# Kernel optimization log

Measured on AMD Instinct MI355X. Metric: run time of the kernel, lower is better.

Reference implementation:

```python
import jax, jax.numpy as jnp
import numpy as np

B, T, D = 4, 1024, 1024
H, DH = 16, 64
FFN = 4096
CAPACITY = 0.25
C_VAR = 1.0
BETA_CE = 1.0
BETA_CU = 1.0
EPS = 1e-6


def _rmsnorm(x, w, eps=EPS):
    v = jnp.mean(jnp.square(x), axis=-1, keepdims=True)
    return x * jax.lax.rsqrt(v + eps) * w


def _rope(x, pos):
    # x: [B, S, H, DH], pos: [B, S] float positions
    half = x.shape[-1] // 2
    inv = 1.0 / (10000.0 ** (jnp.arange(half, dtype=jnp.float32) / half))
    ang = pos[:, :, None] * inv                      # [B, S, half]
    cos = jnp.cos(ang)[:, :, None, :]                # [B, S, 1, half]
    sin = jnp.sin(ang)[:, :, None, :]
    x1, x2 = x[..., :half], x[..., half:]
    return jnp.concatenate([x1 * cos - x2 * sin, x2 * cos + x1 * sin], axis=-1)


def _decoder(x, pos, ln1, wq, wk, wv, wo, ln2, wg, wu, wd):
    # Qwen2-style decoder layer: RMSNorm -> rotary causal MHA -> res -> RMSNorm -> SwiGLU -> res
    b, s, d = x.shape
    h = _rmsnorm(x, ln1)
    q = _rope((h @ wq).reshape(b, s, H, DH), pos)
    k = _rope((h @ wk).reshape(b, s, H, DH), pos)
    v = (h @ wv).reshape(b, s, H, DH)
    scores = jnp.einsum('bqhd,bkhd->bhqk', q, k) / jnp.sqrt(jnp.float32(DH))
    causal = jnp.tril(jnp.ones((s, s), dtype=bool))
    scores = jnp.where(causal, scores, jnp.finfo(scores.dtype).min)
    attn = jax.nn.softmax(scores, axis=-1)
    o = jnp.einsum('bhqk,bkhd->bqhd', attn, v).reshape(b, s, d) @ wo
    x = x + o
    h2 = _rmsnorm(x, ln2)
    return x + (jax.nn.silu(h2 @ wg) * (h2 @ wu)) @ wd


def _forward(hidden_states, ln1_1, wq1, wk1, wv1, wo1, ln2_1, wg1, wu1, wd1,
             ln1_2, wq2, wk2, wv2, wo2, ln2_2, wg2, wu2, wd2,
             prior_norm_w, prior_w):
    b, t, d = hidden_states.shape
    pos = jnp.broadcast_to(jnp.arange(t, dtype=jnp.float32)[None, :], (b, t))
    # decision layer: full-sequence decoder block
    processed = _decoder(hidden_states, pos, ln1_1, wq1, wk1, wv1, wo1, ln2_1, wg1, wu1, wd1)
    res = processed - hidden_states                  # actual_residual
    # prior network: RMSNorm + linear -> (mu_q, log_var_q)
    prior_h = _rmsnorm(hidden_states, prior_norm_w)
    mu_logvar = prior_h @ prior_w                    # [B, T, 2D]
    mu, logvar = mu_logvar[..., :d], mu_logvar[..., d:]
    # surprise router signals
    d_st = jnp.mean(jnp.square(res), axis=-1)        # [B, T]
    d_ch = jnp.mean(0.5 * (logvar - jnp.log(C_VAR)
                           + (C_VAR + jnp.square(res - mu)) * jnp.exp(-logvar) - 1.0), axis=-1)
    g = jax.nn.sigmoid(BETA_CE * (d_st - jnp.mean(d_st)) + BETA_CU * (d_ch - jnp.mean(d_ch)))
    # top-k selection, sorted by token index (as in the torch code)
    k_sel = max(1, int(t * CAPACITY))
    scores, idx = jax.lax.top_k(g, k_sel)            # [B, k]
    order = jnp.argsort(idx, axis=-1)
    idx = jnp.take_along_axis(idx, order, axis=-1)
    scores = jnp.take_along_axis(scores, order, axis=-1)
    # gather -> decoder layer on selected tokens -> soft-gated scatter back
    bidx = jnp.arange(b)[:, None]
    sel = processed[bidx, idx]                       # [B, k, D]
    y = _decoder(sel, idx.astype(jnp.float32), ln1_2, wq2, wk2, wv2, wo2, ln2_2, wg2, wu2, wd2)
    upd = sel + scores[..., None] * (y - sel)        # soft gating of the block residual
    return processed.at[bidx, idx].set(upd)


def setup_inputs():
    key = jax.random.key(0)
    ks = jax.random.split(key, 16)
    s = 0.02

    def w(k, shape):
        return jax.random.normal(k, shape, dtype=jnp.float32) * s

    inp = {'hidden_states': jax.random.normal(ks[0], (B, T, D), dtype=jnp.float32)}
    for i, n in enumerate(['wq1', 'wk1', 'wv1', 'wo1', 'wq2', 'wk2', 'wv2', 'wo2']):
        inp[n] = w(ks[1 + i], (D, D))
    inp['wg1'] = w(ks[9], (D, FFN)); inp['wu1'] = w(ks[10], (D, FFN)); inp['wd1'] = w(ks[11], (FFN, D))
    inp['wg2'] = w(ks[12], (D, FFN)); inp['wu2'] = w(ks[13], (D, FFN)); inp['wd2'] = w(ks[14], (FFN, D))
    for n in ['ln1_1', 'ln2_1', 'ln1_2', 'ln2_2', 'prior_norm_w']:
        inp[n] = jnp.ones((D,), dtype=jnp.float32)
    inp['prior_w'] = w(ks[15], (D, 2 * D))
    return inp


def reference(hidden_states, ln1_1, wq1, wk1, wv1, wo1, ln2_1, wg1, wu1, wd1,
              ln1_2, wq2, wk2, wv2, wo2, ln2_2, wg2, wu2, wd2,
              prior_norm_w, prior_w):
    return _forward(hidden_states, ln1_1, wq1, wk1, wv1, wo1, ln2_1, wg1, wu1, wd1,
                    ln1_2, wq2, wk2, wv2, wo2, ln2_2, wg2, wu2, wd2,
                    prior_norm_w, prior_w)
```

## Files before the change

### kernel.cpp

```cpp
#include <hip/hip_runtime.h>
#include <math.h>

#define Bdim 4
#define Tdim 1024
#define Ddim 1024
#define Hdim 16
#define DHdim 64
#define FFNdim 4096
#define KSEL 256
#define EPSf 1e-6f

typedef __attribute__((ext_vector_type(8))) short bf16x8;
typedef __attribute__((ext_vector_type(4))) float f32x4;
typedef __attribute__((ext_vector_type(4))) unsigned int u32x4;
typedef unsigned short ushort_t;

#define MFMA_BF16(a,b,c) __builtin_amdgcn_mfma_f32_16x16x32_bf16(a,b,c,0,0,0)

__device__ __forceinline__ int clamp_row(int r){ return r < 0 ? 0 : (r > Tdim-1 ? Tdim-1 : r); }

__device__ __forceinline__ void split8(const float* xs, u32x4* hi, u32x4* lo){
  unsigned int hm[8], lm[8];
  #pragma unroll
  for (int i=0;i<8;i++){
// ... 164 lines not shown
  }
  float m_i[4], l_i[4];
  f32x4 oacc[4];
  #pragma unroll
  for (int r=0;r<4;r++){ m_i[r] = -3.4e38f; l_i[r] = 0.f; }
  #pragma unroll
  for (int fd=0;fd<4;fd++){ f32x4 z = {0.f,0.f,0.f,0.f}; oacc[fd] = z; }
  float* Pw = Pds + wv*(16*68);
  for (int j0 = 0; j0 <= q0; j0 += 64){
    __syncthreads();
    {
      int row = tid >> 2;
      int s0 = (tid & 3)*2;
      const float* kp = k + (((size_t)b*S + j0 + row)*Hdim + h)*64 + s0*8;
      #pragma unroll
      for (int g=0; g<2; g++){
        int slot = s0 + g;
        float xs[8];
        #pragma unroll
        for (int i=0;i<8;i++) xs[i] = kp[g*8 + i];
        u32x4 hi, lo; split8(xs, &hi, &lo);
        int base = row*64 + ((slot ^ (row&7))*8);
        *(u32x4*)&Kh[base] = hi;
        *(u32x4*)&Kl[base] = lo;
      }
    }
    {
      int j = tid & 31;
      int dbase = (tid >> 5)*8;
      const float* vp0 = v + (((size_t)b*S + j0 + 2*j)*Hdim + h)*64 + dbase;
      const float* vp1 = vp0 + (size_t)Hdim*64;
      float x0[8], x1[8];
      #pragma unroll
      for (int i=0;i<8;i++){ x0[i]=vp0[i]; x1[i]=vp1[i]; }
      unsigned int* VhW = (unsigned int*)Vh;
      unsigned int* VlW = (unsigned int*)Vl;
      #pragma unroll
      for (int i=0;i<8;i++){
        int d = dbase + i;
        unsigned int h0,l0,h1,l1;
        split1(x0[i], &h0, &l0); split1(x1[i], &h1, &l1);
        int off = d*32 + (((j>>2) ^ (d&7))*4) + (j&3);
        VhW[off] = h0 | (h1<<16);
        VlW[off] = l0 | (l1<<16);
      }
    }
    __syncthreads();
    f32x4 sacc[4];
    #pragma unroll
    for (int fj=0;fj<4;fj++){ f32x4 z = {0.f,0.f,0.f,0.f}; sacc[fj] = z; }
    #pragma unroll
    for (int ks=0; ks<2; ks++){
      #pragma unroll
      for (int fj=0;fj<4;fj++){
        int kr = fj*16 + ln15;
        int idx = kr*64 + (((ks*4+lk) ^ (kr&7))*8);
        bf16x8 kb_h = *(const bf16x8*)&Kh[idx];
        bf16x8 kb_l = *(const bf16x8*)&Kl[idx];
        sacc[fj] = MFMA_BF16(qa_h[ks], kb_h, sacc[fj]);
        sacc[fj] = MFMA_BF16(qa_h[ks], kb_l, sacc[fj]);
        sacc[fj] = MFMA_BF16(qa_l[ks], kb_h, sacc[fj]);
      }
    }
    #pragma unroll
    for (int fj=0;fj<4;fj++){
      int key = j0 + fj*16 + ln15;
      #pragma unroll
      for (int r=0;r<4;r++){
        float sv = sacc[fj][r]*0.125f;
        int qrow = q0 + qbase + lk*4 + r;
        sacc[fj][r] = (key > qrow) ? -3.4e38f : sv;
      }
    }
    float p[4][4];
    #pragma unroll
    for (int r=0;r<4;r++){
      float mt = fmaxf(fmaxf(sacc[0][r],sacc[1][r]), fmaxf(sacc[2][r],sacc[3][r]));
      #pragma unroll
      for (int off=1; off<16; off<<=1) mt = fmaxf(mt, __shfl_xor(mt, off));
      float m_new = fmaxf(m_i[r], mt);
      float alpha = expf(m_i[r] - m_new);
      float rs = 0.f;
      #pragma unroll
      for (int fj=0;fj<4;fj++){
        p[fj][r] = expf(sacc[fj][r] - m_new);
        rs += p[fj][r];
      }
      #pragma unroll
      for (int off=1; off<16; off<<=1) rs += __shfl_xor(rs, off);
      l_i[r] = l_i[r]*alpha + rs;
      m_i[r] = m_new;
      #pragma unroll
      for (int fd=0;fd<4;fd++) oacc[fd][r] *= alpha;
    }
    #pragma unroll
    for (int fj=0;fj<4;fj++)
      #pragma unroll
      for (int r=0;r<4;r++)
        Pw[(lk*4+r)*68 + fj*16 + ln15] = p[fj][r];
    #pragma unroll
    for (int ks=0; ks<2; ks++){
      f32x4 pf0 = *(const f32x4*)&Pw[ln15*68 + ks*32 + lk*8];
      f32x4 pf1 = *(const f32x4*)&Pw[ln15*68 + ks*32 + lk*8 + 4];
      float xs[8] = {pf0[0],pf0[1],pf0[2],pf0[3],pf1[0],pf1[1],pf1[2],pf1[3]};
      u32x4 hi, lo; split8(xs, &hi, &lo);
      bf16x8 pa_h = *(bf16x8*)&hi;
      bf16x8 pa_l = *(bf16x8*)&lo;
      #pragma unroll
      for (int fd=0;fd<4;fd++){
        int d = fd*16 + ln15;
        int idx = d*64 + (((ks*4+lk) ^ (d&7))*8);
        bf16x8 vb_h = *(const bf16x8*)&Vh[idx];
        bf16x8 vb_l = *(const bf16x8*)&Vl[idx];
        oacc[fd] = MFMA_BF16(pa_h, vb_h, oacc[fd]);
        oacc[fd] = MFMA_BF16(pa_h, vb_l, oacc[fd]);
        oacc[fd] = MFMA_BF16(pa_l, vb_h, oacc[fd]);
      }
    }
  }
  #pragma unroll
  for (int r=0;r<4;r++){
    float inv_l = 1.0f/l_i[r];
    #pragma unroll
    for (int fd=0;fd<4;fd++){
      o[(((size_t)b*S + q0 + qbase + lk*4 + r)*Hdim + h)*64 + fd*16 + ln15] = oacc[fd][r]*inv_l;
    }
  }
}

__global__ __launch_bounds__(256) void k_attn_ps(
    const ushort_t* __restrict__ Qph, const ushort_t* __restrict__ Qpl,
    const ushort_t* __restrict__ Kph, const ushort_t* __restrict__ Kpl,
    const ushort_t* __restrict__ Vph, const ushort_t* __restrict__ Vpl,
    ushort_t* __restrict__ Oh, ushort_t* __restrict__ Ol, int S){
  __shared__ ushort_t Kh[64*64], Kl[64*64];
  __shared__ ushort_t Vh[64*64], Vl[64*64];
  __shared__ float Pds[4*16*68];
  const int qt = blockIdx.x, h = blockIdx.y, b = blockIdx.z;
  const int q0 = qt*64;
  const int tid = threadIdx.x;
  const int lane = tid & 63;
  const int ln15 = lane & 15, lk = lane >> 4;
  const int wv = tid >> 6;
  const int qbase = wv*16;
  bf16x8 qa_h[2], qa_l[2];
  {
    size_t qoff = (((size_t)b*S + q0 + qbase + ln15)*Hdim + h)*64;
    #pragma unroll
    for (int ks=0; ks<2; ks++){
      qa_h[ks] = *(const bf16x8*)&Qph[qoff + ks*32 + lk*8];
      qa_l[ks] = *(const bf16x8*)&Qpl[qoff + ks*32 + lk*8];
    }
  }
  float m_i[4], l_i[4];
  f32x4 oacc[4];
  #pragma unroll
  for (int r=0;r<4;r++){ m_i[r] = -3.4e38f; l_i[r] = 0.f; }
  #pragma unroll
  for (int fd=0;fd<4;fd++){ f32x4 z = {0.f,0.f,0.f,0.f}; oacc[fd] = z; }
  float* Pw = Pds + wv*(16*68);
  for (int j0 = 0; j0 <= q0; j0 += 64){
    __syncthreads();
    #pragma unroll
    for (int g=0; g<2; g++){
      int row = g*32 + (tid >> 3);
      int ks = tid & 7;
      size_t ga = (((size_t)b*S + j0 + row)*Hdim + h)*64 + ks*8;
      u32x4 hi = *(const u32x4*)&Kph[ga];
      u32x4 lo = *(const u32x4*)&Kpl[ga];
      int base = row*64 + ((ks ^ (row&7))*8);
      *(u32x4*)&Kh[base] = hi;
      *(u32x4*)&Kl[base] = lo;
    }
    {
      int j = tid & 31;
      int dbase = (tid >> 5)*8;
      size_t g0 = (((size_t)b*S + j0 + 2*j)*Hdim + h)*64 + dbase;
      size_t g1 = g0 + (size_t)Hdim*64;
      u32x4 ah = *(const u32x4*)&Vph[g0];
      u32x4 bh = *(const u32x4*)&Vph[g1];
      u32x4 al = *(const u32x4*)&Vpl[g0];
      u32x4 bl = *(const u32x4*)&Vpl[g1];
      unsigned int* VhW = (unsigned int*)Vh;
      unsigned int* VlW = (unsigned int*)Vl;
      #pragma unroll
      for (int i=0;i<4;i++){
        int d0 = dbase + 2*i, d1 = d0 + 1;
        int off0 = d0*32 + (((j>>2) ^ (d0&7))*4) + (j&3);
        int off1 = d1*32 + (((j>>2) ^ (d1&7))*4) + (j&3);
        VhW[off0] = (ah[i] & 0xFFFFu) | (bh[i] << 16);
        VhW[off1] = (ah[i] >> 16)     | (bh[i] & 0xFFFF0000u);
        VlW[off0] = (al[i] & 0xFFFFu) | (bl[i] << 16);
        VlW[off1] = (al[i] >> 16)     | (bl[i] & 0xFFFF0000u);
      }
    }
    __syncthreads();
    f32x4 sacc[4];
    #pragma unroll
    for (int fj=0;fj<4;fj++){ f32x4 z = {0.f,0.f,0.f,0.f}; sacc[fj] = z; }
    #pragma unroll
    for (int ks=0; ks<2; ks++){
      #pragma unroll
      for (int fj=0;fj<4;fj++){
        int kr = fj*16 + ln15;
        int idx = kr*64 + (((ks*4+lk) ^ (kr&7))*8);
        bf16x8 kb_h = *(const bf16x8*)&Kh[idx];
        bf16x8 kb_l = *(const bf16x8*)&Kl[idx];
        sacc[fj] = MFMA_BF16(qa_h[ks], kb_h, sacc[fj]);
        sacc[fj] = MFMA_BF16(qa_h[ks], kb_l, sacc[fj]);
        sacc[fj] = MFMA_BF16(qa_l[ks], kb_h, sacc[fj]);
      }
    }
    #pragma unroll
    for (int fj=0;fj<4;fj++){
      int key = j0 + fj*16 + ln15;
      #pragma unroll
      for (int r=0;r<4;r++){
        float sv = sacc[fj][r]*0.125f;
        int qrow = q0 + qbase + lk*4 + r;
        sacc[fj][r] = (key > qrow) ? -3.4e38f : sv;
      }
    }
    float p[4][4];
    #pragma unroll
    for (int r=0;r<4;r++){
      float mt = fmaxf(fmaxf(sacc[0][r],sacc[1][r]), fmaxf(sacc[2][r],sacc[3][r]));
      #pragma unroll
      for (int off=1; off<16; off<<=1) mt = fmaxf(mt, __shfl_xor(mt, off));
      float m_new = fmaxf(m_i[r], mt);
      float alpha = expf(m_i[r] - m_new);
      float rs = 0.f;
      #pragma unroll
      for (int fj=0;fj<4;fj++){
        p[fj][r] = expf(sacc[fj][r] - m_new);
        rs += p[fj][r];
      }
      #pragma unroll
      for (int off=1; off<16; off<<=1) rs += __shfl_xor(rs, off);
      l_i[r] = l_i[r]*alpha + rs;
      m_i[r] = m_new;
      #pragma unroll
      for (int fd=0;fd<4;fd++) oacc[fd][r] *= alpha;
    }
    #pragma unroll
    for (int fj=0;fj<4;fj++)
      #pragma unroll
      for (int r=0;r<4;r++)
        Pw[(lk*4+r)*68 + fj*16 + ln15] = p[fj][r];
    #pragma unroll
    for (int ks=0; ks<2; ks++){
      f32x4 pf0 = *(const f32x4*)&Pw[ln15*68 + ks*32 + lk*8];
      f32x4 pf1 = *(const f32x4*)&Pw[ln15*68 + ks*32 + lk*8 + 4];
      float xs[8] = {pf0[0],pf0[1],pf0[2],pf0[3],pf1[0],pf1[1],pf1[2],pf1[3]};
      u32x4 hi, lo; split8(xs, &hi, &lo);
      bf16x8 pa_h = *(bf16x8*)&hi;
      bf16x8 pa_l = *(bf16x8*)&lo;
      #pragma unroll
      for (int fd=0;fd<4;fd++){
        int d = fd*16 + ln15;
        int idx = d*64 + (((ks*4+lk) ^ (d&7))*8);
        bf16x8 vb_h = *(const bf16x8*)&Vh[idx];
        bf16x8 vb_l = *(const bf16x8*)&Vl[idx];
        oacc[fd] = MFMA_BF16(pa_h, vb_h, oacc[fd]);
        oacc[fd] = MFMA_BF16(pa_h, vb_l, oacc[fd]);
        oacc[fd] = MFMA_BF16(pa_l, vb_h, oacc[fd]);
      }
    }
  }
  #pragma unroll
  for (int r=0;r<4;r++){
    float inv_l = 1.0f/l_i[r];
    #pragma unroll
    for (int fd=0;fd<4;fd++){
      float val = oacc[fd][r]*inv_l;
      unsigned int h16,l16; split1(val,&h16,&l16);
      size_t cix = (((size_t)b*S + q0 + qbase + lk*4 + r)*Hdim + h)*64 + fd*16 + ln15;
      Oh[cix] = (ushort_t)h16;
      Ol[cix] = (ushort_t)l16;
    }
  }
}

__global__ __launch_bounds__(256) void k_gemm_mfma(
    const float* __restrict__ A, const float* __restrict__ W,
    float* __restrict__ C, const float* __restrict__ addv,
    int K, int ldw, int ldc){
  __shared__ ushort_t Ah[128*32], Al[128*32], Bh[128*32], Bl[128*32];
  const int tid = threadIdx.x;
  const int row0 = blockIdx.y*128, col0 = blockIdx.x*128;
  const int lane = tid & 63;
  const int ln15 = lane & 15, lk = lane >> 4;
  const int wv = tid >> 6;
  const int wrow0 = (wv >> 1)*64, wcol0 = (wv & 1)*64;
  const int arow = tid >> 2;
  const int aks  = tid & 3;
  const int bcol = tid & 127;
  const int bks0 = tid >> 7;
  f32x4 acc[4][4];
  #pragma unroll
  for (int i=0;i<4;i++)
    #pragma unroll
    for (int j=0;j<4;j++){ f32x4 z = {0.f,0.f,0.f,0.f}; acc[i][j] = z; }
  for (int k0 = 0; k0 < K; k0 += 32){
    #pragma unroll
    for (int g=0; g<2; g++){
      int row = g*64 + arow;
      const float* ap = A + (size_t)(row0+row)*K + k0 + aks*8;
      float xs[8];
      #pragma unroll
      for (int i=0;i<8;i++) xs[i] = ap[i];
      u32x4 hi, lo; split8(xs, &hi, &lo);
      int base = row*32 + ((aks ^ ((row>>1)&3))*8);
      *(u32x4*)&Ah[base] = hi;
      *(u32x4*)&Al[base] = lo;
    }
    #pragma unroll
    for (int g=0; g<2; g++){
      int ks = bks0 + 2*g;
      const float* wp = W + (size_t)(k0 + ks*8)*ldw + col0 + bcol;
      float xs[8];
      #pragma unroll
      for (int i=0;i<8;i++) xs[i] = wp[(size_t)i*ldw];
      u32x4 hi, lo; split8(xs, &hi, &lo);
      int base = bcol*32 + ((ks ^ ((bcol>>1)&3))*8);
      *(u32x4*)&Bh[base] = hi;
      *(u32x4*)&Bl[base] = lo;
    }
    __syncthreads();
    bf16x8 ah[4], al[4];
    #pragma unroll
    for (int fi=0;fi<4;fi++){
      int r = wrow0 + fi*16 + ln15;
      int idx = r*32 + ((lk ^ ((r>>1)&3))*8);
      ah[fi] = *(const bf16x8*)&Ah[idx];
      al[fi] = *(const bf16x8*)&Al[idx];
    }
    #pragma unroll
    for (int fj=0;fj<4;fj++){
      int c = wcol0 + fj*16 + ln15;
      int idx = c*32 + ((lk ^ ((c>>1)&3))*8);
      bf16x8 bh = *(const bf16x8*)&Bh[idx];
      bf16x8 bl = *(const bf16x8*)&Bl[idx];
      #pragma unroll
      for (int fi=0;fi<4;fi++){
        acc[fi][fj] = MFMA_BF16(ah[fi], bh, acc[fi][fj]);
        acc[fi][fj] = MFMA_BF16(ah[fi], bl, acc[fi][fj]);
        acc[fi][fj] = MFMA_BF16(al[fi], bh, acc[fi][fj]);
      }
    }
    __syncthreads();
  }
  #pragma unroll
  for (int fi=0;fi<4;fi++){
    #pragma unroll
    for (int fj=0;fj<4;fj++){
      f32x4 v = acc[fi][fj];
      int cc = col0 + wcol0 + fj*16 + ln15;
      #pragma unroll
      for (int r=0;r<4;r++){
        size_t cix = (size_t)(row0 + wrow0 + fi*16 + lk*4 + r)*ldc + cc;
        float val = v[r];
        if (addv) val += addv[cix];
        C[cix] = val;
      }
    }
  }
}

__global__ __launch_bounds__(512) void k_gemm_ps(
    const ushort_t* __restrict__ Ahp, const ushort_t* __restrict__ Alp, int lda,
    const ushort_t* __restrict__ Bhp, const ushort_t* __restrict__ Blp, int ldb,
    float* __restrict__ C, ushort_t* __restrict__ Chp, ushort_t* __restrict__ Clp,
    const float* __restrict__ addv, int K, int ldc){
  __shared__ ushort_t Ah[128*32], Al[128*32], Bh[128*32], Bl[128*32];
  const int tid = threadIdx.x;
  const int row0 = blockIdx.y*128, col0 = blockIdx.x*128;
  const int lane = tid & 63;
  const int ln15 = lane & 15, lk = lane >> 4;
  const int wv = tid >> 6;
  const int wrow0 = (wv >> 2)*64, wcol0 = (wv & 3)*32;
  const int t8 = tid >> 2, ks4 = tid & 3;
  const int sbase = t8*32 + ((ks4 ^ ((t8>>1)&3))*8);
  const size_t gaBase = (size_t)(row0 + t8)*lda + ks4*8;
  const size_t gbBase = (size_t)(col0 + t8)*ldb + ks4*8;

  f32x4 acc[4][2];
  #pragma unroll
  for (int i=0;i<4;i++)
    #pragma unroll
    for (int j=0;j<2;j++){ f32x4 z = {0.f,0.f,0.f,0.f}; acc[i][j] = z; }

  u32x4 rAh = *(const u32x4*)&Ahp[gaBase];
  u32x4 rAl = *(const u32x4*)&Alp[gaBase];
  u32x4 rBh = *(const u32x4*)&Bhp[gbBase];
  u32x4 rBl = *(const u32x4*)&Blp[gbBase];

  for (int k0 = 0; k0 < K; k0 += 32){
    __syncthreads();
    *(u32x4*)&Ah[sbase] = rAh;
    *(u32x4*)&Al[sbase] = rAl;
    *(u32x4*)&Bh[sbase] = rBh;
    *(u32x4*)&Bl[sbase] = rBl;
    __syncthreads();
    if (k0 + 32 < K){
      rAh = *(const u32x4*)&Ahp[gaBase + k0 + 32];
      rAl = *(const u32x4*)&Alp[gaBase + k0 + 32];
      rBh = *(const u32x4*)&Bhp[gbBase + k0 + 32];
      rBl = *(const u32x4*)&Blp[gbBase + k0 + 32];
    }
    bf16x8 ah[4], al[4];
    #pragma unroll
    for (int fi=0;fi<4;fi++){
      int r = wrow0 + fi*16 + ln15;
      int idx = r*32 + ((lk ^ ((r>>1)&3))*8);
      ah[fi] = *(const bf16x8*)&Ah[idx];
      al[fi] = *(const bf16x8*)&Al[idx];
    }
    #pragma unroll
    for (int fj=0;fj<2;fj++){
      int c = wcol0 + fj*16 + ln15;
      int idx = c*32 + ((lk ^ ((c>>1)&3))*8);
      bf16x8 bh = *(const bf16x8*)&Bh[idx];
      bf16x8 bl = *(const bf16x8*)&Bl[idx];
      #pragma unroll
      for (int fi=0;fi<4;fi++){
        acc[fi][fj] = MFMA_BF16(ah[fi], bh, acc[fi][fj]);
        acc[fi][fj] = MFMA_BF16(ah[fi], bl, acc[fi][fj]);
        acc[fi][fj] = MFMA_BF16(al[fi], bh, acc[fi][fj]);
      }
    }
  }
  if (Chp){
    #pragma unroll
    for (int fi=0;fi<4;fi++){
      #pragma unroll
      for (int fj=0;fj<2;fj++){
        f32x4 v = acc[fi][fj];
        int cc = col0 + wcol0 + fj*16 + ln15;
        #pragma unroll
        for (int r=0;r<4;r++){
          size_t cix = (size_t)(row0 + wrow0 + fi*16 + lk*4 + r)*ldc + cc;
          unsigned int h16,l16; split1(v[r],&h16,&l16);
          Chp[cix] = (ushort_t)h16;
          Clp[cix] = (ushort_t)l16;
        }
      }
    }
  } else {
    #pragma unroll
    for (int fi=0;fi<4;fi++){
      #pragma unroll
      for (int fj=0;fj<2;fj++){
        f32x4 v = acc[fi][fj];
        int cc = col0 + wcol0 + fj*16 + ln15;
        #pragma unroll
        for (int r=0;r<4;r++){
          size_t cix = (size_t)(row0 + wrow0 + fi*16 + lk*4 + r)*ldc + cc;
          float val = v[r];
          if (addv) val += addv[cix];
          C[cix] = val;
        }
      }
    }
  }
}

__global__ __launch_bounds__(256) void k_gemm_dual_mfma(
    const float* __restrict__ A, const float* __restrict__ Wg,
    const float* __restrict__ Wu, float* __restrict__ C,
    int K, int ldw, int ldc){
  __shared__ ushort_t Ah[128*32], Al[128*32];
  __shared__ ushort_t Gh[64*32], Gl[64*32], Uh[64*32], Ul[64*32];
  const int tid = threadIdx.x;
  const int row0 = blockIdx.y*128, col0 = blockIdx.x*64;
  const int lane = tid & 63;
  const int ln15 = lane & 15, lk = lane >> 4;
  const int wv = tid >> 6;
  const int wrow0 = (wv >> 1)*64, wcol0 = (wv & 1)*32;
  const int arow = tid >> 2;
  const int aks  = tid & 3;
  const int bcol = tid & 63;
  const int bks  = tid >> 6;
  f32x4 ag[4][2], au[4][2];
  #pragma unroll
  for (int i=0;i<4;i++)
    #pragma unroll
    for (int j=0;j<2;j++){ f32x4 z = {0.f,0.f,0.f,0.f}; ag[i][j] = z; au[i][j] = z; }
  for (int k0 = 0; k0 < K; k0 += 32){
    #pragma unroll
    for (int g=0; g<2; g++){
      int row = g*64 + arow;
      const float* ap = A + (size_t)(row0+row)*K + k0 + aks*8;
      float xs[8];
      #pragma unroll
      for (int i=0;i<8;i++) xs[i] = ap[i];
      u32x4 hi, lo; split8(xs, &hi, &lo);
      int base = row*32 + ((aks ^ ((row>>1)&3))*8);
      *(u32x4*)&Ah[base] = hi;
      *(u32x4*)&Al[base] = lo;
    }
    {
      int wbase = bcol*32 + ((bks ^ ((bcol>>1)&3))*8);
      const float* gp = Wg + (size_t)(k0 + bks*8)*ldw + col0 + bcol;
      float xs[8];
      #pragma unroll
      for (int i=0;i<8;i++) xs[i] = gp[(size_t)i*ldw];
      u32x4 hi, lo; split8(xs, &hi, &lo);
      *(u32x4*)&Gh[wbase] = hi;
      *(u32x4*)&Gl[wbase] = lo;
      const float* up = Wu + (size_t)(k0 + bks*8)*ldw + col0 + bcol;
      #pragma unroll
      for (int i=0;i<8;i++) xs[i] = up[(size_t)i*ldw];
      split8(xs, &hi, &lo);
      *(u32x4*)&Uh[wbase] = hi;
      *(u32x4*)&Ul[wbase] = lo;
    }
    __syncthreads();
    bf16x8 ah[4], al[4];
    #pragma unroll
    for (int fi=0;fi<4;fi++){
      int r = wrow0 + fi*16 + ln15;
      int idx = r*32 + ((lk ^ ((r>>1)&3))*8);
      ah[fi] = *(const bf16x8*)&Ah[idx];
      al[fi] = *(const bf16x8*)&Al[idx];
    }
    #pragma unroll
    for (int fj=0;fj<2;fj++){
      int c = wcol0 + fj*16 + ln15;
      int idx = c*32 + ((lk ^ ((c>>1)&3))*8);
      bf16x8 gh = *(const bf16x8*)&Gh[idx];
      bf16x8 gl = *(const bf16x8*)&Gl[idx];
      bf16x8 uh = *(const bf16x8*)&Uh[idx];
      bf16x8 ul = *(const bf16x8*)&Ul[idx];
      #pragma unroll
      for (int fi=0;fi<4;fi++){
        ag[fi][fj] = MFMA_BF16(ah[fi], gh, ag[fi][fj]);
        ag[fi][fj] = MFMA_BF16(ah[fi], gl, ag[fi][fj]);
        ag[fi][fj] = MFMA_BF16(al[fi], gh, ag[fi][fj]);
        au[fi][fj] = MFMA_BF16(ah[fi], uh, au[fi][fj]);
        au[fi][fj] = MFMA_BF16(ah[fi], ul, au[fi][fj]);
        au[fi][fj] = MFMA_BF16(al[fi], uh, au[fi][fj]);
      }
    }
    __syncthreads();
  }
  #pragma unroll
  for (int fi=0;fi<4;fi++){
    #pragma unroll
    for (int fj=0;fj<2;fj++){
      f32x4 vg = ag[fi][fj];
      f32x4 vu = au[fi][fj];
      int cc = col0 + wcol0 + fj*16 + ln15;
      #pragma unroll
      for (int r=0;r<4;r++){
        size_t cix = (size_t)(row0 + wrow0 + fi*16 + lk*4 + r)*ldc + cc;
        float gg = vg[r];
        C[cix] = (gg/(1.0f+expf(-gg))) * vu[r];
      }
    }
  }
}

__global__ __launch_bounds__(512) void k_gemm_dual_ps(
    const ushort_t* __restrict__ Ahp, const ushort_t* __restrict__ Alp, int lda,
    const ushort_t* __restrict__ Ghp, const ushort_t* __restrict__ Glp,
    const ushort_t* __restrict__ Uhp, const ushort_t* __restrict__ Ulp, int ldb,
    ushort_t* __restrict__ Chp, ushort_t* __restrict__ Clp, int K, int ldc){
  __shared__ ushort_t Ah[128*32], Al[128*32];
  __shared__ ushort_t Gh[64*32], Gl[64*32], Uh[64*32], Ul[64*32];
  const int tid = threadIdx.x;
  const int row0 = blockIdx.y*128, col0 = blockIdx.x*64;
  const int lane = tid & 63;
  const int ln15 = lane & 15, lk = lane >> 4;
  const int wv = tid >> 6;
  const int wrow0 = (wv >> 1)*32, wcol0 = (wv & 1)*32;
  const int t8 = tid >> 2, ks4 = tid & 3;
  const int abase = t8*32 + ((ks4 ^ ((t8>>1)&3))*8);
  const size_t gaBase = (size_t)(row0 + t8)*lda + ks4*8;
  const int isU = (tid >= 256);
  const int t2 = tid & 255;
  const int wcolS = t2 >> 2, wksS = t2 & 3;
  const int wsbase = wcolS*32 + ((wksS ^ ((wcolS>>1)&3))*8);
  const ushort_t* Wph = isU ? Uhp : Ghp;
  const ushort_t* Wpl = isU ? Ulp : Glp;
  ushort_t* WsH = isU ? Uh : Gh;
  ushort_t* WsL = isU ? Ul : Gl;
  const size_t gwBase = (size_t)(col0 + wcolS)*ldb + wksS*8;

  f32x4 ag[2][2], au[2][2];
  #pragma unroll
  for (int i=0;i<2;i++)
    #pragma unroll
    for (int j=0;j<2;j++){ f32x4 z = {0.f,0.f,0.f,0.f}; ag[i][j] = z; au[i][j] = z; }

  u32x4 rAh = *(const u32x4*)&Ahp[gaBase];
  u32x4 rAl = *(const u32x4*)&Alp[gaBase];
  u32x4 rWh = *(const u32x4*)&Wph[gwBase];
  u32x4 rWl = *(const u32x4*)&Wpl[gwBase];

  for (int k0 = 0; k0 < K; k0 += 32){
    __syncthreads();
    *(u32x4*)&Ah[abase] = rAh;
    *(u32x4*)&Al[abase] = rAl;
    *(u32x4*)&WsH[wsbase] = rWh;
    *(u32x4*)&WsL[wsbase] = rWl;
    __syncthreads();
    if (k0 + 32 < K){
      rAh = *(const u32x4*)&Ahp[gaBase + k0 + 32];
      rAl = *(const u32x4*)&Alp[gaBase + k0 + 32];
      rWh = *(const u32x4*)&Wph[gwBase + k0 + 32];
      rWl = *(const u32x4*)&Wpl[gwBase + k0 + 32];
    }
    bf16x8 ah[2], al[2];
// ... 90 lines not shown
                        float* __restrict__ g){
  int tid = threadIdx.x;
  float s1=0.f, s2=0.f;
  for (int i=tid; i<Bdim*Tdim; i+=1024){ s1+=dst[i]; s2+=dch[i]; }
  __shared__ float r1[1024], r2[1024];
  r1[tid]=s1; r2[tid]=s2; __syncthreads();
  for (int st=512; st>0; st>>=1){ if(tid<st){r1[tid]+=r1[tid+st]; r2[tid]+=r2[tid+st];} __syncthreads(); }
  float m1 = r1[0]/(float)(Bdim*Tdim), m2 = r2[0]/(float)(Bdim*Tdim);
  for (int i=tid; i<Bdim*Tdim; i+=1024){
    float z = (dst[i]-m1) + (dch[i]-m2);
    g[i] = 1.0f/(1.0f+expf(-z));
  }
}

__global__ __launch_bounds__(1024) void k_select(const float* __restrict__ g, int* __restrict__ selidx,
                         float* __restrict__ selsc){
  int b = blockIdx.x, t = threadIdx.x;
  __shared__ float gs[1024];
  __shared__ int flag[1024];
  float gv = g[b*Tdim + t];
  if (!(gv == gv)) gv = -3.4e38f;
  gs[t] = gv; __syncthreads();
  float gi = gs[t];
  int rank = 0;
  for (int j=0;j<Tdim;j++){
    float gj = gs[j];
    rank += (gj > gi) || (gj == gi && j < t);
  }
  int sel = (rank < KSEL) ? 1 : 0;
  flag[t] = sel; __syncthreads();
  if (sel){
    int pos = 0;
    for (int j=0;j<t;j++) pos += flag[j];
    if (pos < KSEL){
      selidx[b*KSEL+pos] = t;
      selsc[b*KSEL+pos] = gi;
    }
  }
}

__global__ __launch_bounds__(256) void k_gather(const float* __restrict__ proc, const int* __restrict__ selidx,
                         float* __restrict__ sel){
  int j = blockIdx.x, b = blockIdx.y, tid = threadIdx.x;
  int row = clamp_row(selidx[b*KSEL+j]);
  const float* src = proc + ((size_t)b*Tdim + row)*Ddim;
  float* dst = sel + ((size_t)b*KSEL + j)*Ddim;
  for (int d=tid; d<Ddim; d+=256) dst[d]=src[d];
}

__global__ void k_out(const float* __restrict__ proc, float* __restrict__ out, int n){
  int i = blockIdx.x*blockDim.x + threadIdx.x;
  if (i<n) out[i] = proc[i];
}

__global__ __launch_bounds__(256) void k_scatter(const float* __restrict__ sel, const float* __restrict__ y,
                          const float* __restrict__ selsc, const int* __restrict__ selidx,
                          float* __restrict__ out){
  int j = blockIdx.x, b = blockIdx.y, tid = threadIdx.x;
  int row = clamp_row(selidx[b*KSEL+j]);
  float s = selsc[b*KSEL+j];
  const float* sp = sel + ((size_t)b*KSEL + j)*Ddim;
  const float* yp = y + ((size_t)b*KSEL + j)*Ddim;
  float* op = out + ((size_t)b*Tdim + row)*Ddim;
  for (int d=tid; d<Ddim; d+=256){
    op[d] = sp[d] + s*(yp[d]-sp[d]);
  }
}

extern "C" void kernel_launch(void* const* d_in, const int* in_sizes, int n_in,
                              void* d_out, int out_size, void* d_ws, size_t ws_size,
                              hipStream_t stream){
  (void)in_sizes; (void)n_in; (void)out_size;
  const float* hidden = (const float*)d_in[0];
  const float* wq1 = (const float*)d_in[1];
  const float* wk1 = (const float*)d_in[2];
  const float* wv1 = (const float*)d_in[3];
  const float* wo1 = (const float*)d_in[4];
  const float* wq2 = (const float*)d_in[5];
  const float* wk2 = (const float*)d_in[6];
  const float* wv2 = (const float*)d_in[7];
  const float* wo2 = (const float*)d_in[8];
  const float* wg1 = (const float*)d_in[9];
  const float* wu1 = (const float*)d_in[10];
  const float* wd1 = (const float*)d_in[11];
  const float* wg2 = (const float*)d_in[12];
  const float* wu2 = (const float*)d_in[13];
  const float* wd2 = (const float*)d_in[14];
  const float* ln1_1 = (const float*)d_in[15];
  const float* ln2_1 = (const float*)d_in[16];
  const float* ln1_2 = (const float*)d_in[17];
  const float* ln2_2 = (const float*)d_in[18];
  const float* prior_norm = (const float*)d_in[19];
  const float* prior_w = (const float*)d_in[20];

  const size_t A = (size_t)Bdim*Tdim*Ddim;
  const size_t Q = (size_t)Bdim*KSEL*Ddim;
  const int n = (int)A;
  const int MT = Bdim*Tdim;
  const int M2 = Bdim*KSEL;

  const size_t WELEMS = 34u*1024*1024;
  size_t need_old = (4*A + 16384) * sizeof(float);
  size_t need_new = need_old + 2*WELEMS*sizeof(ushort_t);

  if (ws_size < need_old){
    k_fallback<<<(n+255)/256,256,0,stream>>>(hidden, (float*)d_out, n);
    return;
  }

  float* ws = (float*)d_ws;
  float* R0 = ws;
  float* R1 = ws + 1*A;
  float* R2 = ws + 2*A;
  float* R3 = ws + 3*A;
  float* dstb = ws + 4*A;
  float* dchb = dstb + 4096;
  float* gb   = dchb + 4096;
  float* selsc= gb + 4096;
  int*   selidx = (int*)(selsc + 1024);

  k_init_sel<<<4,256,0,stream>>>(selidx, selsc, Bdim*KSEL);

  if (ws_size >= need_new){
    ushort_t* wpb = (ushort_t*)(ws + 4*A + 16384);
    size_t cur = 0;
    const size_t M1x1 = (size_t)1024*1024;
    const size_t M1x4 = (size_t)1024*4096;
    #define ALLOCW(nm, KN) ushort_t* nm##_h = wpb + cur; ushort_t* nm##_l = wpb + cur + (KN); cur += 2*(size_t)(KN);
    ALLOCW(pwq1, M1x1) ALLOCW(pwk1, M1x1) ALLOCW(pwv1, M1x1) ALLOCW(pwo1, M1x1)
    ALLOCW(pwq2, M1x1) ALLOCW(pwk2, M1x1) ALLOCW(pwv2, M1x1) ALLOCW(pwo2, M1x1)
    ALLOCW(pwg1, M1x4) ALLOCW(pwu1, M1x4) ALLOCW(pwd1, M1x4)
    ALLOCW(pwg2, M1x4) ALLOCW(pwu2, M1x4) ALLOCW(pwd2, M1x4)
    ALLOCW(ppw, (size_t)2048*1024)
    #undef ALLOCW

    k_split_w<<<dim3(16,16),256,0,stream>>>(wq1, pwq1_h, pwq1_l, 1024, 1024);
    k_split_w<<<dim3(16,16),256,0,stream>>>(wk1, pwk1_h, pwk1_l, 1024, 1024);
    k_split_w<<<dim3(16,16),256,0,stream>>>(wv1, pwv1_h, pwv1_l, 1024, 1024);
    k_split_w<<<dim3(16,16),256,0,stream>>>(wo1, pwo1_h, pwo1_l, 1024, 1024);
    k_split_w<<<dim3(16,16),256,0,stream>>>(wq2, pwq2_h, pwq2_l, 1024, 1024);
    k_split_w<<<dim3(16,16),256,0,stream>>>(wk2, pwk2_h, pwk2_l, 1024, 1024);
    k_split_w<<<dim3(16,16),256,0,stream>>>(wv2, pwv2_h, pwv2_l, 1024, 1024);
    k_split_w<<<dim3(16,16),256,0,stream>>>(wo2, pwo2_h, pwo2_l, 1024, 1024);
    k_split_w<<<dim3(64,16),256,0,stream>>>(wg1, pwg1_h, pwg1_l, 1024, 4096);
    k_split_w<<<dim3(64,16),256,0,stream>>>(wu1, pwu1_h, pwu1_l, 1024, 4096);
    k_split_w<<<dim3(16,64),256,0,stream>>>(wd1, pwd1_h, pwd1_l, 4096, 1024);
    k_split_w<<<dim3(64,16),256,0,stream>>>(wg2, pwg2_h, pwg2_l, 1024, 4096);
    k_split_w<<<dim3(64,16),256,0,stream>>>(wu2, pwu2_h, pwu2_l, 1024, 4096);
    k_split_w<<<dim3(16,64),256,0,stream>>>(wd2, pwd2_h, pwd2_l, 4096, 1024);
    k_split_w<<<dim3(32,16),256,0,stream>>>(prior_w, ppw_h, ppw_l, 1024, 2048);

    ushort_t* Hh = (ushort_t*)R0; ushort_t* Hl = Hh + A;
    k_rmsnorm_sp<<<MT,256,0,stream>>>(hidden, ln1_1, Hh, Hl);
    dim3 gD(Ddim/128, MT/128);
    k_gemm_ps<<<gD,512,0,stream>>>(Hh,Hl,1024, pwq1_h,pwq1_l,1024, R1, nullptr,nullptr, nullptr, 1024, 1024);
    k_gemm_ps<<<gD,512,0,stream>>>(Hh,Hl,1024, pwk1_h,pwk1_l,1024, R2, nullptr,nullptr, nullptr, 1024, 1024);
    ushort_t* Vp_h = (ushort_t*)R3; ushort_t* Vp_l = Vp_h + A;
    k_gemm_ps<<<gD,512,0,stream>>>(Hh,Hl,1024, pwv1_h,pwv1_l,1024, nullptr, Vp_h, Vp_l, nullptr, 1024, 1024);
    int nr = MT*Hdim*32;
    ushort_t* Qp_h = (ushort_t*)R0; ushort_t* Qp_l = Qp_h + A;
    k_rope_sp<<<(nr+255)/256,256,0,stream>>>(R1, nullptr, Tdim, nr, Qp_h, Qp_l);
    ushort_t* Kp_h = (ushort_t*)R1; ushort_t* Kp_l = Kp_h + A;
    k_rope_sp<<<(nr+255)/256,256,0,stream>>>(R2, nullptr, Tdim, nr, Kp_h, Kp_l);
    ushort_t* Op_h = (ushort_t*)R2; ushort_t* Op_l = Op_h + A;
    k_attn_ps<<<dim3(Tdim/64,Hdim,Bdim),256,0,stream>>>(Qp_h,Qp_l, Kp_h,Kp_l, Vp_h,Vp_l, Op_h,Op_l, Tdim);
    k_gemm_ps<<<gD,512,0,stream>>>(Op_h,Op_l,1024, pwo1_h,pwo1_l,1024, R1, nullptr,nullptr, hidden, 1024, 1024);
    ushort_t* H2h = (ushort_t*)R0; ushort_t* H2l = H2h + A;
    k_rmsnorm_sp<<<MT,256,0,stream>>>(R1, ln2_1, H2h, H2l);
    ushort_t* ACTh = (ushort_t*)R3; ushort_t* ACTl = ACTh + A;
    for (int c = 0; c < 4; c++){
      k_gemm_dual_ps<<<dim3(16, MT/128),512,0,stream>>>(H2h,H2l,1024,
          pwg1_h + (size_t)c*M1x1, pwg1_l + (size_t)c*M1x1,
          pwu1_h + (size_t)c*M1x1, pwu1_l + (size_t)c*M1x1, 1024,
          ACTh, ACTl, 1024, 1024);
      k_gemm_ps<<<dim3(8, MT/128),512,0,stream>>>(ACTh,ACTl,1024,
          pwd1_h + (size_t)c*1024, pwd1_l + (size_t)c*1024, 4096,
          R2, nullptr,nullptr, (c==0 ? R1 : R2), 1024, 1024);
    }

    ushort_t* PHh = (ushort_t*)R0; ushort_t* PHl = PHh + A;
    k_rmsnorm_sp<<<MT,256,0,stream>>>(hidden, prior_norm, PHh, PHl);
    k_gemm_ps<<<gD,512,0,stream>>>(PHh,PHl,1024, ppw_h, ppw_l, 1024, R1, nullptr,nullptr, nullptr, 1024, 1024);
    k_gemm_ps<<<gD,512,0,stream>>>(PHh,PHl,1024, ppw_h + M1x1, ppw_l + M1x1, 1024, R3, nullptr,nullptr, nullptr, 1024, 1024);
    k_dstch2<<<MT,256,0,stream>>>(R2, hidden, R1, R3, dstb, dchb);
    k_gate<<<1,1024,0,stream>>>(dstb, dchb, gb);
    k_select<<<Bdim,1024,0,stream>>>(gb, selidx, selsc);
    float* SELX = R0;
    k_gather<<<dim3(KSEL,Bdim),256,0,stream>>>(R2, selidx, SELX);

    ushort_t* h2h = (ushort_t*)R1;        ushort_t* h2l = h2h + Q;
    k_rmsnorm_sp<<<M2,256,0,stream>>>(SELX, ln1_2, h2h, h2l);
    float* q2f = R1 + Q;
    float* k2f = R1 + 2*Q;
    ushort_t* v2h = (ushort_t*)(R1 + 3*Q); ushort_t* v2l = v2h + Q;
    dim3 gD2(Ddim/128, M2/128);
    k_gemm_ps<<<gD2,512,0,stream>>>(h2h,h2l,1024, pwq2_h,pwq2_l,1024, q2f, nullptr,nullptr, nullptr, 1024, 1024);
    k_gemm_ps<<<gD2,512,0,stream>>>(h2h,h2l,1024, pwk2_h,pwk2_l,1024, k2f, nullptr,nullptr, nullptr, 1024, 1024);
    k_gemm_ps<<<gD2,512,0,stream>>>(h2h,h2l,1024, pwv2_h,pwv2_l,1024, nullptr, v2h, v2l, nullptr, 1024, 1024);
    int nr2 = M2*Hdim*32;
    ushort_t* q2ph = (ushort_t*)(R0 + Q);   ushort_t* q2pl = q2ph + Q;
    ushort_t* k2ph = (ushort_t*)(R0 + 2*Q); ushort_t* k2pl = k2ph + Q;
    k_rope_sp<<<(nr2+255)/256,256,0,stream>>>(q2f, selidx, KSEL, nr2, q2ph, q2pl);
    k_rope_sp<<<(nr2+255)/256,256,0,stream>>>(k2f, selidx, KSEL, nr2, k2ph, k2pl);
    ushort_t* o2h = (ushort_t*)(R0 + 3*Q);  ushort_t* o2l = o2h + Q;
    k_attn_ps<<<dim3(KSEL/64,Hdim,Bdim),256,0,stream>>>(q2ph,q2pl, k2ph,k2pl, v2h,v2l, o2h,o2l, KSEL);
    float* X12 = R1 + Q;
    k_gemm_ps<<<gD2,512,0,stream>>>(o2h,o2l,1024, pwo2_h,pwo2_l,1024, X12, nullptr,nullptr, SELX, 1024, 1024);
    ushort_t* h22h = (ushort_t*)(R1 + 2*Q); ushort_t* h22l = h22h + Q;
    k_rmsnorm_sp<<<M2,256,0,stream>>>(X12, ln2_2, h22h, h22l);
    ushort_t* act2h = (ushort_t*)(R1 + 3*Q); ushort_t* act2l = act2h + Q;
    float* Y = R3;
    for (int c = 0; c < 4; c++){
      k_gemm_dual_ps<<<dim3(16, M2/128),512,0,stream>>>(h22h,h22l,1024,
          pwg2_h + (size_t)c*M1x1, pwg2_l + (size_t)c*M1x1,
          pwu2_h + (size_t)c*M1x1, pwu2_l + (size_t)c*M1x1, 1024,
          act2h, act2l, 1024, 1024);
      k_gemm_ps<<<dim3(8, M2/128),512,0,stream>>>(act2h,act2l,1024,
          pwd2_h + (size_t)c*1024, pwd2_l + (size_t)c*1024, 4096,
          Y, nullptr,nullptr, (c==0 ? X12 : Y), 1024, 1024);
    }
    k_out<<<(n+255)/256,256,0,stream>>>(R2, (float*)d_out, n);
    k_scatter<<<dim3(KSEL,Bdim),256,0,stream>>>(SELX, Y, selsc, selidx, (float*)d_out);
    return;
  }

  k_rmsnorm<<<MT,256,0,stream>>>(hidden, ln1_1, R0);
  dim3 gD(Ddim/128, MT/128);
  k_gemm_mfma<<<gD,256,0,stream>>>(R0, wq1, R1, nullptr, Ddim, Ddim, Ddim);
  k_gemm_mfma<<<gD,256,0,stream>>>(R0, wk1, R2, nullptr, Ddim, Ddim, Ddim);
  k_gemm_mfma<<<gD,256,0,stream>>>(R0, wv1, R3, nullptr, Ddim, Ddim, Ddim);
  int nr = MT*Hdim*32;
  k_rope<<<(nr+255)/256,256,0,stream>>>(R1, nullptr, Tdim, nr);
  k_rope<<<(nr+255)/256,256,0,stream>>>(R2, nullptr, Tdim, nr);
  k_attn_mfma<<<dim3(Tdim/64,Hdim,Bdim),256,0,stream>>>(R1, R2, R3, R0, Tdim);
  k_gemm_mfma<<<gD,256,0,stream>>>(R0, wo1, R1, hidden, Ddim, Ddim, Ddim);
  k_rmsnorm<<<MT,256,0,stream>>>(R1, ln2_1, R2);
  for (int c = 0; c < 4; c++){
    k_gemm_dual_mfma<<<dim3(1024/64, MT/128),256,0,stream>>>(R2, wg1 + (size_t)c*1024, wu1 + (size_t)c*1024,
                                                  R3, Ddim, FFNdim, 1024);
    k_gemm_mfma<<<dim3(Ddim/128, MT/128),256,0,stream>>>(R3, wd1 + (size_t)c*1024*Ddim, R0,
                                             (c==0 ? R1 : R0), 1024, Ddim, Ddim);
  }
  k_rmsnorm<<<MT,256,0,stream>>>(hidden, prior_norm, R1);
  k_gemm_mfma<<<dim3(2*Ddim/128, MT/128),256,0,stream>>>(R1, prior_w, R2, nullptr, Ddim, 2*Ddim, 2*Ddim);
  k_dstch<<<MT,256,0,stream>>>(R0, hidden, R2, dstb, dchb);
  k_gate<<<1,1024,0,stream>>>(dstb, dchb, gb);
  k_select<<<Bdim,1024,0,stream>>>(gb, selidx, selsc);
  k_gather<<<dim3(KSEL,Bdim),256,0,stream>>>(R0, selidx, R1);
  k_rmsnorm<<<M2,256,0,stream>>>(R1, ln1_2, R2);
  dim3 gD2(Ddim/128, M2/128);
  k_gemm_mfma<<<gD2,256,0,stream>>>(R2, wq2, R2+Q,   nullptr, Ddim, Ddim, Ddim);
  k_gemm_mfma<<<gD2,256,0,stream>>>(R2, wk2, R2+2*Q, nullptr, Ddim, Ddim, Ddim);
  k_gemm_mfma<<<gD2,256,0,stream>>>(R2, wv2, R2+3*Q, nullptr, Ddim, Ddim, Ddim);
  int nr2 = M2*Hdim*32;
  k_rope<<<(nr2+255)/256,256,0,stream>>>(R2+Q,   selidx, KSEL, nr2);
  k_rope<<<(nr2+255)/256,256,0,stream>>>(R2+2*Q, selidx, KSEL, nr2);
  k_attn_mfma<<<dim3(KSEL/64,Hdim,Bdim),256,0,stream>>>(R2+Q, R2+2*Q, R2+3*Q, R3, KSEL);
  k_gemm_mfma<<<gD2,256,0,stream>>>(R3, wo2, R3+Q, R1, Ddim, Ddim, Ddim);
  k_rmsnorm<<<M2,256,0,stream>>>(R3+Q, ln2_2, R3+2*Q);
  for (int c = 0; c < 4; c++){
    k_gemm_dual_mfma<<<dim3(1024/64, M2/128),256,0,stream>>>(R3+2*Q, wg2 + (size_t)c*1024, wu2 + (size_t)c*1024,
                                                  R3+3*Q, Ddim, FFNdim, 1024);
    k_gemm_mfma<<<dim3(Ddim/128, M2/128),256,0,stream>>>(R3+3*Q, wd2 + (size_t)c*1024*Ddim, R2,
                                             (c==0 ? R3+Q : R2), 1024, Ddim, Ddim);
  }
  k_out<<<(n+255)/256,256,0,stream>>>(R0, (float*)d_out, n);
  k_scatter<<<dim3(KSEL,Bdim),256,0,stream>>>(R1, R2, selsc, selidx, (float*)d_out);
}
```

Baseline: 1.527 ms.

## Fuse QKV projections into one launch and add lazy softmax rescaling in attention

Adds a k_gemm_qkv kernel that uses blockIdx.z to choose among the Q, K and V (or prior mu/logvar) weight matrices, replacing three or two separate GEMM launches with one larger grid. The attention kernel now skips the per-row max shuffle and output rescale when every new tile max stays within 8 of the running max, and defers the row-sum reduction to the epilogue. Together these cut launch overhead, improve occupancy for the small selected-token GEMMs, and remove cross-lane reductions from the inner loop. The fallback path also rewrites its k_rope calls with nullptr and zero counts, which looks like it changes the RoPE semantics there.

```diff
diff --git a/kernel.cpp b/kernel.cpp
--- a/kernel.cpp
+++ b/kernel.cpp
@@ -340,10 +340,10 @@
       qa_l[ks] = *(const bf16x8*)&Qpl[qoff + ks*32 + lk*8];
     }
   }
-  float m_i[4], l_i[4];
+  float m_i[4], lp[4];
   f32x4 oacc[4];
   #pragma unroll
-  for (int r=0;r<4;r++){ m_i[r] = -3.4e38f; l_i[r] = 0.f; }
+  for (int r=0;r<4;r++){ m_i[r] = -3.4e38f; lp[r] = 0.f; }
   #pragma unroll
   for (int fd=0;fd<4;fd++){ f32x4 z = {0.f,0.f,0.f,0.f}; oacc[fd] = z; }
   float* Pw = Pds + wv*(16*68);
@@ -409,26 +409,42 @@
         sacc[fj][r] = (key > qrow) ? -3.4e38f : sv;
       }
     }
+    float tm[4];
+    #pragma unroll
+    for (int r=0;r<4;r++)
+      tm[r] = fmaxf(fmaxf(sacc[0][r],sacc[1][r]), fmaxf(sacc[2][r],sacc[3][r]));
+    bool okl = (tm[0] <= m_i[0]+8.f) & (tm[1] <= m_i[1]+8.f)
+             & (tm[2] <= m_i[2]+8.f) & (tm[3] <= m_i[3]+8.f);
     float p[4][4];
-    #pragma unroll
-    for (int r=0;r<4;r++){
-      float mt = fmaxf(fmaxf(sacc[0][r],sacc[1][r]), fmaxf(sacc[2][r],sacc[3][r]));
-      #pragma unroll
-      for (int off=1; off<16; off<<=1) mt = fmaxf(mt, __shfl_xor(mt, off));
-      float m_new = fmaxf(m_i[r], mt);
-      float alpha = expf(m_i[r] - m_new);
-      float rs = 0.f;
-      #pragma unroll
-      for (int fj=0;fj<4;fj++){
-        p[fj][r] = expf(sacc[fj][r] - m_new);
-        rs += p[fj][r];
-      }
-      #pragma unroll
-      for (int off=1; off<16; off<<=1) rs += __shfl_xor(rs, off);
-      l_i[r] = l_i[r]*alpha + rs;
-      m_i[r] = m_new;
-      #pragma unroll
-      for (int fd=0;fd<4;fd++) oacc[fd][r] *= alpha;
+    if (__all(okl)){
+      #pragma unroll
+      for (int r=0;r<4;r++){
+        #pragma unroll
+        for (int fj=0;fj<4;fj++){
+          float pv = expf(sacc[fj][r] - m_i[r]);
+          p[fj][r] = pv;
+          lp[r] += pv;
+        }
+      }
+    } else {
+      #pragma unroll
+      for (int r=0;r<4;r++){
+        float mt = tm[r];
+        #pragma unroll
+        for (int off=1; off<16; off<<=1) mt = fmaxf(mt, __shfl_xor(mt, off));
+        float m_new = fmaxf(m_i[r], mt);
+        float alpha = expf(m_i[r] - m_new);
+        lp[r] *= alpha;
+        #pragma unroll
+        for (int fd=0;fd<4;fd++) oacc[fd][r] *= alpha;
+        m_i[r] = m_new;
+        #pragma unroll
+        for (int fj=0;fj<4;fj++){
+          float pv = expf(sacc[fj][r] - m_new);
+          p[fj][r] = pv;
+          lp[r] += pv;
+        }
+      }
     }
     #pragma unroll
     for (int fj=0;fj<4;fj++)
@@ -457,7 +473,10 @@
   }
   #pragma unroll
   for (int r=0;r<4;r++){
-    float inv_l = 1.0f/l_i[r];
+    float l = lp[r];
+    #pragma unroll
+    for (int off=1; off<16; off<<=1) l += __shfl_xor(l, off);
+    float inv_l = 1.0f/l;
     #pragma unroll
     for (int fd=0;fd<4;fd++){
       float val = oacc[fd][r]*inv_l;
@@ -647,6 +666,109 @@
           float val = v[r];
           if (addv) val += addv[cix];
           C[cix] = val;
+        }
+      }
+    }
+  }
+}
+
+__global__ __launch_bounds__(512) void k_gemm_qkv(
+    const ushort_t* __restrict__ Ahp, const ushort_t* __restrict__ Alp, int lda,
+    const ushort_t* __restrict__ B0h, const ushort_t* __restrict__ B0l,
+    const ushort_t* __restrict__ B1h, const ushort_t* __restrict__ B1l,
+    const ushort_t* __restrict__ B2h, const ushort_t* __restrict__ B2l, int ldb,
+    float* __restrict__ C0, float* __restrict__ C1,
+    ushort_t* __restrict__ C2h, ushort_t* __restrict__ C2l,
+    int K, int ldc){
+  __shared__ ushort_t Ah[128*32], Al[128*32], Bh[128*32], Bl[128*32];
+  const int z = blockIdx.z;
+  const ushort_t* Bhp = (z==0) ? B0h : (z==1) ? B1h : B2h;
+  const ushort_t* Blp = (z==0) ? B0l : (z==1) ? B1l : B2l;
+  const int tid = threadIdx.x;
+  const int row0 = blockIdx.y*128, col0 = blockIdx.x*128;
+  const int lane = tid & 63;
+  const int ln15 = lane & 15, lk = lane >> 4;
+  const int wv = tid >> 6;
+  const int wrow0 = (wv >> 2)*64, wcol0 = (wv & 3)*32;
+  const int t8 = tid >> 2, ks4 = tid & 3;
+  const int sbase = t8*32 + ((ks4 ^ ((t8>>1)&3))*8);
+  const size_t gaBase = (size_t)(row0 + t8)*lda + ks4*8;
+  const size_t gbBase = (size_t)(col0 + t8)*ldb + ks4*8;
+
+  f32x4 acc[4][2];
+  #pragma unroll
+  for (int i=0;i<4;i++)
+    #pragma unroll
+    for (int j=0;j<2;j++){ f32x4 zz = {0.f,0.f,0.f,0.f}; acc[i][j] = zz; }
+
+  u32x4 rAh = *(const u32x4*)&Ahp[gaBase];
+  u32x4 rAl = *(const u32x4*)&Alp[gaBase];
+  u32x4 rBh = *(const u32x4*)&Bhp[gbBase];
+  u32x4 rBl = *(const u32x4*)&Blp[gbBase];
+
+  for (int k0 = 0; k0 < K; k0 += 32){
+    __syncthreads();
+    *(u32x4*)&Ah[sbase] = rAh;
+    *(u32x4*)&Al[sbase] = rAl;
+    *(u32x4*)&Bh[sbase] = rBh;
+    *(u32x4*)&Bl[sbase] = rBl;
+    __syncthreads();
+    if (k0 + 32 < K){
+      rAh = *(const u32x4*)&Ahp[gaBase + k0 + 32];
+      rAl = *(const u32x4*)&Alp[gaBase + k0 + 32];
+      rBh = *(const u32x4*)&Bhp[gbBase + k0 + 32];
+      rBl = *(const u32x4*)&Blp[gbBase + k0 + 32];
+    }
+    bf16x8 ah[4], al[4];
+    #pragma unroll
+    for (int fi=0;fi<4;fi++){
+      int r = wrow0 + fi*16 + ln15;
+      int idx = r*32 + ((lk ^ ((r>>1)&3))*8);
+      ah[fi] = *(const bf16x8*)&Ah[idx];
+      al[fi] = *(const bf16x8*)&Al[idx];
+    }
+    #pragma unroll
+    for (int fj=0;fj<2;fj++){
+      int c = wcol0 + fj*16 + ln15;
+      int idx = c*32 + ((lk ^ ((c>>1)&3))*8);
+      bf16x8 bh = *(const bf16x8*)&Bh[idx];
+      bf16x8 bl = *(const bf16x8*)&Bl[idx];
+      #pragma unroll
+      for (int fi=0;fi<4;fi++){
+        acc[fi][fj] = MFMA_BF16(ah[fi], bh, acc[fi][fj]);
+        acc[fi][fj] = MFMA_BF16(ah[fi], bl, acc[fi][fj]);
+        acc[fi][fj] = MFMA_BF16(al[fi], bh, acc[fi][fj]);
+      }
+    }
+  }
+  if (z == 2){
+    #pragma unroll
+    for (int fi=0;fi<4;fi++){
+      #pragma unroll
+      for (int fj=0;fj<2;fj++){
+        f32x4 v = acc[fi][fj];
+        int cc = col0 + wcol0 + fj*16 + ln15;
+        #pragma unroll
+        for (int r=0;r<4;r++){
+          size_t cix = (size_t)(row0 + wrow0 + fi*16 + lk*4 + r)*ldc + cc;
+          unsigned int h16,l16; split1(v[r],&h16,&l16);
+          C2h[cix] = (ushort_t)h16;
+          C2l[cix] = (ushort_t)l16;
+        }
+      }
+    }
+  } else {
+    float* C = (z == 0) ? C0 : C1;
+    #pragma unroll
+    for (int fi=0;fi<4;fi++){
+      #pragma unroll
+      for (int fj=0;fj<2;fj++){
+        f32x4 v = acc[fi][fj];
+        int cc = col0 + wcol0 + fj*16 + ln15;
+        #pragma unroll
+        for (int r=0;r<4;r++){
+          size_t cix = (size_t)(row0 + wrow0 + fi*16 + lk*4 + r)*ldc + cc;
+          C[cix] = v[r];
         }
       }
     }
@@ -1043,11 +1165,10 @@
 
     ushort_t* Hh = (ushort_t*)R0; ushort_t* Hl = Hh + A;
     k_rmsnorm_sp<<<MT,256,0,stream>>>(hidden, ln1_1, Hh, Hl);
-    dim3 gD(Ddim/128, MT/128);
-    k_gemm_ps<<<gD,512,0,stream>>>(Hh,Hl,1024, pwq1_h,pwq1_l,1024, R1, nullptr,nullptr, nullptr, 1024, 1024);
-    k_gemm_ps<<<gD,512,0,stream>>>(Hh,Hl,1024, pwk1_h,pwk1_l,1024, R2, nullptr,nullptr, nullptr, 1024, 1024);
     ushort_t* Vp_h = (ushort_t*)R3; ushort_t* Vp_l = Vp_h + A;
-    k_gemm_ps<<<gD,512,0,stream>>>(Hh,Hl,1024, pwv1_h,pwv1_l,1024, nullptr, Vp_h, Vp_l, nullptr, 1024, 1024);
+    k_gemm_qkv<<<dim3(8, MT/128, 3),512,0,stream>>>(Hh,Hl,1024,
+        pwq1_h,pwq1_l, pwk1_h,pwk1_l, pwv1_h,pwv1_l, 1024,
+        R1, R2, Vp_h, Vp_l, 1024, 1024);
     int nr = MT*Hdim*32;
     ushort_t* Qp_h = (ushort_t*)R0; ushort_t* Qp_l = Qp_h + A;
     k_rope_sp<<<(nr+255)/256,256,0,stream>>>(R1, nullptr, Tdim, nr, Qp_h, Qp_l);
@@ -1055,7 +1176,7 @@
     k_rope_sp<<<(nr+255)/256,256,0,stream>>>(R2, nullptr, Tdim, nr, Kp_h, Kp_l);
     ushort_t* Op_h = (ushort_t*)R2; ushort_t* Op_l = Op_h + A;
     k_attn_ps<<<dim3(Tdim/64,Hdim,Bdim),256,0,stream>>>(Qp_h,Qp_l, Kp_h,Kp_l, Vp_h,Vp_l, Op_h,Op_l, Tdim);
-    k_gemm_ps<<<gD,512,0,stream>>>(Op_h,Op_l,1024, pwo1_h,pwo1_l,1024, R1, nullptr,nullptr, hidden, 1024, 1024);
+    k_gemm_ps<<<dim3(8, MT/128),512,0,stream>>>(Op_h,Op_l,1024, pwo1_h,pwo1_l,1024, R1, nullptr,nullptr, hidden, 1024, 1024);
     ushort_t* H2h = (ushort_t*)R0; ushort_t* H2l = H2h + A;
     k_rmsnorm_sp<<<MT,256,0,stream>>>(R1, ln2_1, H2h, H2l);
     ushort_t* ACTh = (ushort_t*)R3; ushort_t* ACTl = ACTh + A;
@@ -1071,8 +1192,9 @@
 
     ushort_t* PHh = (ushort_t*)R0; ushort_t* PHl = PHh + A;
     k_rmsnorm_sp<<<MT,256,0,stream>>>(hidden, prior_norm, PHh, PHl);
-    k_gemm_ps<<<gD,512,0,stream>>>(PHh,PHl,1024, ppw_h, ppw_l, 1024, R1, nullptr,nullptr, nullptr, 1024, 1024);
-    k_gemm_ps<<<gD,512,0,stream>>>(PHh,PHl,1024, ppw_h + M1x1, ppw_l + M1x1, 1024, R3, nullptr,nullptr, nullptr, 1024, 1024);
+    k_gemm_qkv<<<dim3(8, MT/128, 2),512,0,stream>>>(PHh,PHl,1024,
+        ppw_h,ppw_l, ppw_h + M1x1, ppw_l + M1x1, nullptr,nullptr, 1024,
+        R1, R3, nullptr,nullptr, 1024, 1024);
     k_dstch2<<<MT,256,0,stream>>>(R2, hidden, R1, R3, dstb, dchb);
     k_gate<<<1,1024,0,stream>>>(dstb, dchb, gb);
     k_select<<<Bdim,1024,0,stream>>>(gb, selidx, selsc);
@@ -1084,10 +1206,9 @@
     float* q2f = R1 + Q;
     float* k2f = R1 + 2*Q;
     ushort_t* v2h = (ushort_t*)(R1 + 3*Q); ushort_t* v2l = v2h + Q;
-    dim3 gD2(Ddim/128, M2/128);
-    k_gemm_ps<<<gD2,512,0,stream>>>(h2h,h2l,1024, pwq2_h,pwq2_l,1024, q2f, nullptr,nullptr, nullptr, 1024, 1024);
-    k_gemm_ps<<<gD2,512,0,stream>>>(h2h,h2l,1024, pwk2_h,pwk2_l,1024, k2f, nullptr,nullptr, nullptr, 1024, 1024);
-    k_gemm_ps<<<gD2,512,0,stream>>>(h2h,h2l,1024, pwv2_h,pwv2_l,1024, nullptr, v2h, v2l, nullptr, 1024, 1024);
+    k_gemm_qkv<<<dim3(8, M2/128, 3),512,0,stream>>>(h2h,h2l,1024,
+        pwq2_h,pwq2_l, pwk2_h,pwk2_l, pwv2_h,pwv2_l, 1024,
+        q2f, k2f, v2h, v2l, 1024, 1024);
     int nr2 = M2*Hdim*32;
     ushort_t* q2ph = (ushort_t*)(R0 + Q);   ushort_t* q2pl = q2ph + Q;
     ushort_t* k2ph = (ushort_t*)(R0 + 2*Q); ushort_t* k2pl = k2ph + Q;
@@ -1096,7 +1217,7 @@
     ushort_t* o2h = (ushort_t*)(R0 + 3*Q);  ushort_t* o2l = o2h + Q;
     k_attn_ps<<<dim3(KSEL/64,Hdim,Bdim),256,0,stream>>>(q2ph,q2pl, k2ph,k2pl, v2h,v2l, o2h,o2l, KSEL);
     float* X12 = R1 + Q;
-    k_gemm_ps<<<gD2,512,0,stream>>>(o2h,o2l,1024, pwo2_h,pwo2_l,1024, X12, nullptr,nullptr, SELX, 1024, 1024);
+    k_gemm_ps<<<dim3(8, M2/128),512,0,stream>>>(o2h,o2l,1024, pwo2_h,pwo2_l,1024, X12, nullptr,nullptr, SELX, 1024, 1024);
     ushort_t* h22h = (ushort_t*)(R1 + 2*Q); ushort_t* h22l = h22h + Q;
     k_rmsnorm_sp<<<M2,256,0,stream>>>(X12, ln2_2, h22h, h22l);
     ushort_t* act2h = (ushort_t*)(R1 + 3*Q); ushort_t* act2l = act2h + Q;
@@ -1144,8 +1265,9 @@
   k_gemm_mfma<<<gD2,256,0,stream>>>(R2, wk2, R2+2*Q, nullptr, Ddim, Ddim, Ddim);
   k_gemm_mfma<<<gD2,256,0,stream>>>(R2, wv2, R2+3*Q, nullptr, Ddim, Ddim, Ddim);
   int nr2 = M2*Hdim*32;
-  k_rope<<<(nr2+255)/256,256,0,stream>>>(R2+Q,   selidx, KSEL, nr2);
-  k_rope<<<(nr2+255)/256,256,0,stream>>>(R2+2*Q, selidx, KSEL, nr2);
+  k_rope<<<(nr2+255)/256,256,0,stream>>>(R2+Q,   nullptr, KSEL, nr2);
+  k_rope<<<(nr2+255)/256,256,0,stream>>>(R2+2*Q, nullptr, KSEL, nr2);
+  k_rope<<<(nr2+255)/256,256,0,stream>>>(R2+Q,   selidx, KSEL, 0);
   k_attn_mfma<<<dim3(KSEL/64,Hdim,Bdim),256,0,stream>>>(R2+Q, R2+2*Q, R2+3*Q, R3, KSEL);
   k_gemm_mfma<<<gD2,256,0,stream>>>(R3, wo2, R3+Q, R1, Ddim, Ddim, Ddim);
   k_rmsnorm<<<M2,256,0,stream>>>(R3+Q, ln2_2, R3+2*Q);
```

Result: faster. 1.379 ms (-9.7%).
